# Kernel tuning notes

Measured on AMD Instinct MI355X. Metric: run time of the kernel, lower is better.

Reference implementation:

```python
import jax, jax.numpy as jnp
import numpy as np

N_NODES = 100000
N_EDGES = 1600000
NFEAT = 128
NHID = 128
NCLASS = 40


def gcn_conv(x, W, b, src, dst, n_nodes):
    """PyG-style GCNConv: x' = D^{-1/2}(A+I)D^{-1/2} (x W) + b."""
    h = x @ W  # [N, out]
    loop = jnp.arange(n_nodes, dtype=src.dtype)
    s = jnp.concatenate([src, loop])  # add self-loops
    d = jnp.concatenate([dst, loop])
    deg = jax.ops.segment_sum(jnp.ones_like(s, dtype=h.dtype), d, num_segments=n_nodes)
    dinv = jnp.where(deg > 0, jax.lax.rsqrt(deg), 0.0)
    norm = dinv[s] * dinv[d]  # [E+N]
    msg = h[s] * norm[:, None]  # gather + scale
    out = jax.ops.segment_sum(msg, d, num_segments=n_nodes)  # scatter-add
    return out + b


def setup_inputs() -> dict:
    key = jax.random.key(0)
    ks = jax.random.split(key, 6)
    x = jax.random.normal(ks[0], (N_NODES, NFEAT), dtype=jnp.float32)
    edge_index = jax.random.randint(ks[1], (2, N_EDGES), 0, N_NODES, dtype=jnp.int64)
    sc1 = 1.0 / np.sqrt(NFEAT)
    sc2 = 1.0 / np.sqrt(NHID)
    W1 = jax.random.normal(ks[2], (NFEAT, NHID), dtype=jnp.float32) * sc1
    b1 = jnp.zeros((NHID,), dtype=jnp.float32)
    Wm = jax.random.normal(ks[3], (NHID, NHID), dtype=jnp.float32) * sc2
    bm = jnp.zeros((NHID,), dtype=jnp.float32)
    W2 = jax.random.normal(ks[4], (NHID, NCLASS), dtype=jnp.float32) * sc2
    b2 = jnp.zeros((NCLASS,), dtype=jnp.float32)
    return {"x": x, "edge_index": edge_index, "W1": W1, "b1": b1,
            "Wm": Wm, "bm": bm, "W2": W2, "b2": b2}


def reference(x, edge_index, W1, b1, Wm, bm, W2, b2):
    # StandGCNX forward, eval mode (dropout = identity)
    src, dst = edge_index[0], edge_index[1]
    n = x.shape[0]
    h = jax.nn.relu(gcn_conv(x, W1, b1, src, dst, n))
    h = jax.nn.relu(gcn_conv(h, Wm, bm, src, dst, n))
    out = gcn_conv(h, W2, b2, src, dst, n)
    return out
```

## Files before the change

kernel.cpp:

```cpp
#include <hip/hip_runtime.h>
#include <hip/hip_bf16.h>

typedef __attribute__((ext_vector_type(8))) short bf16x8;
typedef __attribute__((ext_vector_type(4))) float f32x4;

__device__ __forceinline__ ushort bf16rne(float f) {
    uint u = __float_as_uint(f);
    return (ushort)((u + 0x7fffu + ((u >> 16) & 1u)) >> 16);
}
__device__ __forceinline__ void unpack2(uint p, float& a, float& b) {
    a = __uint_as_float(p << 16);
    b = __uint_as_float(p & 0xffff0000u);
}


__global__ __launch_bounds__(256) void k_pre1(const float* __restrict__ W1,
                                              const float* __restrict__ Wm,
                                              const float* __restrict__ W2,
                                              ushort* __restrict__ w1t,
                                              ushort* __restrict__ wmt,
                                              ushort* __restrict__ w2t,
                                              const int* __restrict__ dst,
                                              int* __restrict__ bcnt, int E) {
    __shared__ int hist[512];
    int b = blockIdx.x;
    int t = threadIdx.x;
    if (b < 152) {
        if (b < 64) {
            int i = b * 256 + t; int k = i >> 7, n = i & 127;
            w1t[n * 128 + k] = bf16rne(W1[k * 128 + n]);
        } else if (b < 128) {
            int i = (b - 64) * 256 + t; int k = i >> 7, n = i & 127;
            wmt[n * 128 + k] = bf16rne(Wm[k * 128 + n]);
        } else {
            int i = (b - 128) * 256 + t;
            if (i < 6144) {
                int n = i >> 7, k = i & 127;
                w2t[n * 128 + k] = (n < 40) ? bf16rne(W2[k * 40 + n]) : (ushort)0;
            }
        }
        return;
    }
    hist[t] = 0; hist[t + 256] = 0;
    __syncthreads();
    int off = (b - 152) * 4096;
    int cnt = min(4096, E - off);
    for (int i = t; i < cnt; i += 256) atomicAdd(&hist[dst[off + i] >> 8], 1);
    __syncthreads();
    if (hist[t]) atomicAdd(&bcnt[t], hist[t]);
    if (hist[t + 256]) atomicAdd(&bcnt[t + 256], hist[t + 256]);
}

__global__ void k_bscan(const int* __restrict__ bcnt, int* __restrict__ bbase,
                        int* __restrict__ bcur, int nbuck) {
    __shared__ int s[512];
    int t = threadIdx.x;
    s[t] = (t < nbuck) ? bcnt[t] : 0;
    __syncthreads();
    for (int d = 1; d < 512; d <<= 1) {
        int u = (t >= d) ? s[t - d] : 0;
        __syncthreads();
        if (t >= d) s[t] += u;
        __syncthreads();
    }
    int excl = (t == 0) ? 0 : s[t - 1];
    bbase[t] = excl;
    if (t < nbuck) bcur[t] = excl;
    if (t == 511) bbase[512] = s[511];
}


__global__ __launch_bounds__(256) void k_pack_gemm(const int* __restrict__ src,
                                                   const int* __restrict__ dst,
                                                   int* __restrict__ bcur,
                                                   uint* __restrict__ pairbuf,
                                                   int E, int nbuck, int ntile,
                                                   const float* __restrict__ A,
                                                   const ushort* __restrict__ Wt,
                                                   ushort* __restrict__ C, int M) {
    __shared__ int hist[512];
    __shared__ int scn[512];
    __shared__ int cur[512];
    __shared__ int gbase[512];
    __shared__ uint sorted[4096];
    int t = threadIdx.x;
    if ((int)blockIdx.x >= ntile) {
        int blk = blockIdx.x - ntile;
        int wave = t >> 6, lane = t & 63;
        int m16 = lane & 15, quad = lane >> 4;
        int rowA = blk * 64 + wave * 16 + m16;
        int rA = min(rowA, M - 1);
        const float4* A4 = (const float4*)A;

        f32x4 acc[8];
#pragma unroll
        for (int i = 0; i < 8; i++) acc[i] = (f32x4){0.f, 0.f, 0.f, 0.f};
#pragma unroll
        for (int it = 0; it < 4; it++) {
            float4 f0 = A4[(size_t)rA * 32 + 8 * it + 2 * quad];
            float4 f1 = A4[(size_t)rA * 32 + 8 * it + 2 * quad + 1];
            bf16x8 af;
            af[0] = (short)bf16rne(f0.x); af[1] = (short)bf16rne(f0.y);
            af[2] = (short)bf16rne(f0.z); af[3] = (short)bf16rne(f0.w);
            af[4] = (short)bf16rne(f1.x); af[5] = (short)bf16rne(f1.y);
            af[6] = (short)bf16rne(f1.z); af[7] = (short)bf16rne(f1.w);
#pragma unroll
            for (int nt = 0; nt < 8; nt++) {
                bf16x8 bfr = *(const bf16x8*)(Wt + (size_t)(nt * 16 + m16) * 128 + it * 32 + quad * 8);
                acc[nt] = __builtin_amdgcn_mfma_f32_16x16x32_bf16(af, bfr, acc[nt], 0, 0, 0);
            }
        }
        int rowBase = blk * 64 + wave * 16 + quad * 4;
#pragma unroll
        for (int nt = 0; nt < 8; nt++) {
            int col = nt * 16 + m16;
#pragma unroll
            for (int r = 0; r < 4; r++) {
                int row = rowBase + r;
                if (row < M) C[(size_t)row * 128 + col] = bf16rne(acc[nt][r]);
            }
        }
        return;
    }
    int off = blockIdx.x * 4096;
    int cnt = min(4096, E - off);
    hist[t] = 0; hist[t + 256] = 0;
    __syncthreads();
    for (int i = t; i < cnt; i += 256) {
        int b = dst[off + i] >> 8;
        atomicAdd(&hist[b], 1);
    }
    __syncthreads();
    scn[t] = hist[t]; scn[t + 256] = hist[t + 256];
    __syncthreads();
    for (int d = 1; d < 256; d <<= 1) {
        int u0 = (t >= d) ? scn[t - d] : 0;
        int u1 = (t >= d) ? scn[256 + t - d] : 0;
        __syncthreads();
        if (t >= d) { scn[t] += u0; scn[256 + t] += u1; }
        __syncthreads();
    }
    int tot0 = scn[255];
    scn[256 + t] += tot0;
    __syncthreads();
    cur[t] = (t == 0) ? 0 : scn[t - 1];
    cur[t + 256] = scn[t + 255];
    if (t < nbuck && hist[t] > 0) gbase[t] = atomicAdd(&bcur[t], hist[t]);
    int t2 = t + 256;
    if (t2 < nbuck && hist[t2] > 0) gbase[t2] = atomicAdd(&bcur[t2], hist[t2]);
    __syncthreads();
    for (int i = t; i < cnt; i += 256) {
        int d = dst[off + i];
        int s = src[off + i];
        int b = d >> 8;
        int pos = atomicAdd(&cur[b], 1);
        sorted[pos] = ((uint)(d & 255) << 24) | (uint)s;
    }
    __syncthreads();
    int wid = t >> 6, lane = t & 63;
    for (int b = wid; b < nbuck; b += 4) {
        int n = hist[b];
        if (n == 0) continue;
        int ls = (b == 0) ? 0 : scn[b - 1];
        int gb = gbase[b];
        for (int j = lane; j < n; j += 64)
            pairbuf[gb + j] = sorted[ls + j];
    }
}

#define CSR_CAP 5632
__global__ __launch_bounds__(256) void k_csrbuild(const uint* __restrict__ pairbuf,
                                                  const int* __restrict__ bbase,
                                                  int* __restrict__ rowptr,
                                                  float* __restrict__ dinv,
                                                  int* __restrict__ csr,
                                                  int N, int nbuck) {
    __shared__ int lhist[256];
    __shared__ int scn[256];
    __shared__ int lcur[256];
    __shared__ int lcsr[CSR_CAP];
    int b = blockIdx.x;
    int base = b << 8;
    int nn = min(256, N - base);
    int lo = bbase[b], hi = bbase[b + 1];
    int cnt = hi - lo;
    int t = threadIdx.x;
    lhist[t] = 0;
    __syncthreads();
    for (int i = t; i < cnt; i += 256) atomicAdd(&lhist[pairbuf[lo + i] >> 24], 1);
    __syncthreads();
    int mydeg = lhist[t];
    scn[t] = mydeg;
    __syncthreads();
    for (int d = 1; d < 256; d <<= 1) {
        int u = (t >= d) ? scn[t - d] : 0;
        __syncthreads();
        if (t >= d) scn[t] += u;
        __syncthreads();
    }
    int excl = (t == 0) ? 0 : scn[t - 1];
    lcur[t] = excl;
    if (t < nn) {
        rowptr[base + t] = lo + excl;
        dinv[base + t] = rsqrtf((float)(mydeg + 1));
    }
    if (b == nbuck - 1 && t == 0) rowptr[N] = hi;
    __syncthreads();
    if (cnt <= CSR_CAP) {
        for (int i = t; i < cnt; i += 256) {
            uint p = pairbuf[lo + i];
            int pos = atomicAdd(&lcur[p >> 24], 1);
            lcsr[pos] = (int)(p & 0xFFFFFFu);
        }
        __syncthreads();
        for (int i = t; i < cnt; i += 256) csr[lo + i] = lcsr[i];
    } else {
        for (int i = t; i < cnt; i += 256) {
            uint p = pairbuf[lo + i];
            int pos = lo + atomicAdd(&lcur[p >> 24], 1);
            csr[pos] = (int)(p & 0xFFFFFFu);
        }
    }
}


template <bool EDGE_W>
__device__ __forceinline__ void agg_issue8(const uint* __restrict__ g32, int lane,
                                           int sidx, int swi, int j,
                                           uint P[8], float W[8]) {
#pragma unroll
    for (int k = 0; k < 8; k++) {
        int s = __builtin_amdgcn_readlane(sidx, j + k);
        W[k] = __int_as_float(__builtin_amdgcn_readlane(swi, j + k));
        P[k] = g32[(size_t)s * 64 + lane];
    }
}
__device__ __forceinline__ void agg_consume8(const uint P[8], const float W[8],
                                             float& a0, float& a1) {
#pragma unroll
    for (int k = 0; k < 8; k++) {
        float u, v;
        unpack2(P[k], u, v);
        a0 += u * W[k];
        a1 += v * W[k];
    }
}

template <int NT, bool EDGE_W>
__device__ __forceinline__ void fused_agg_gemm(const ushort* __restrict__ g,
                                               const float* __restrict__ dinv,
                                               const int* __restrict__ rowptr,
                                               const int* __restrict__ csr,
                                               const float* __restrict__ bias,
                                               const ushort* __restrict__ Wt,
                                               ushort* __restrict__ C,
                                               int M, int ccols) {
    __shared__ ushort hs[32][136];
    __shared__ int nextNode;
    int t = threadIdx.x;
    if (t == 0) nextNode = 0;
    __syncthreads();
    int lane = t & 63;
    const uint* g32 = (const uint*)g;
    float2 bb = ((const float2*)bias)[lane];

    for (;;) {
        int idx0 = 0;
        if (lane == 0) idx0 = atomicAdd(&nextNode, 2);
        idx0 = __builtin_amdgcn_readfirstlane(idx0);
        if (idx0 >= 32) break;
        int ndA = min(blockIdx.x * 32 + idx0, M - 1);
        int ndB = min(blockIdx.x * 32 + idx0 + 1, M - 1);
        float dnA = dinv[ndA], dnB = dinv[ndB];
        int e0A = rowptr[ndA], e1A = rowptr[ndA + 1];
        int e0B = rowptr[ndB], e1B = rowptr[ndB + 1];
        uint pSA = g32[(size_t)ndA * 64 + lane];
        uint pSB = g32[(size_t)ndB * 64 + lane];
        float a0, a1, b0, b1;
        {
            float u, v;
            unpack2(pSA, u, v);
            if (EDGE_W) { a0 = u * dnA; a1 = v * dnA; } else { a0 = u; a1 = v; }
            unpack2(pSB, u, v);
            if (EDGE_W) { b0 = u * dnB; b1 = v * dnB; } else { b0 = u; b1 = v; }
        }
        int baseA = e0A, baseB = e0B;
        while (baseA < e1A || baseB < e1B) {
            int ncA = e1A - baseA; if (ncA > 64) ncA = 64;
            int ncB = e1B - baseB; if (ncB > 64) ncB = 64;
            int sidxA = 0, swiA = 0, sidxB = 0, swiB = 0;
            if (lane < ncA) {
                sidxA = csr[baseA + lane];
                swiA = EDGE_W ? __float_as_int(dinv[sidxA]) : 0x3f800000;
            }
            if (lane < ncB) {
                sidxB = csr[baseB + lane];
                swiB = EDGE_W ? __float_as_int(dinv[sidxB]) : 0x3f800000;
            }
            int nc8A = (ncA + 7) & ~7;
            int nc8B = (ncB + 7) & ~7;
            int jA = 0, jB = 0;
            while (jA < nc8A && jB < nc8B) {
                uint PA[8], PB[8];
                float WA[8], WB[8];
                agg_issue8<EDGE_W>(g32, lane, sidxA, swiA, jA, PA, WA);
                agg_issue8<EDGE_W>(g32, lane, sidxB, swiB, jB, PB, WB);
                agg_consume8(PA, WA, a0, a1);
                agg_consume8(PB, WB, b0, b1);
                jA += 8; jB += 8;
            }
            while (jA < nc8A) {
                uint PA[8]; float WA[8];
                agg_issue8<EDGE_W>(g32, lane, sidxA, swiA, jA, PA, WA);
                agg_consume8(PA, WA, a0, a1);
                jA += 8;
            }
            while (jB < nc8B) {
                uint PB[8]; float WB[8];
                agg_issue8<EDGE_W>(g32, lane, sidxB, swiB, jB, PB, WB);
                agg_consume8(PB, WB, b0, b1);
                jB += 8;
            }
            baseA += ncA;
            baseB += ncB;
        }
        float o0 = fmaxf(a0 * dnA + bb.x, 0.f);
        float o1 = fmaxf(a1 * dnA + bb.y, 0.f);
        float o2 = fmaxf(b0 * dnB + bb.x, 0.f);
        float o3 = fmaxf(b1 * dnB + bb.y, 0.f);
        uint qA = (uint)bf16rne(o0) | ((uint)bf16rne(o1) << 16);
        uint qB = (uint)bf16rne(o2) | ((uint)bf16rne(o3) << 16);
        *(uint*)&hs[idx0][lane * 2] = qA;
        *(uint*)&hs[idx0 + 1][lane * 2] = qB;
    }
    __syncthreads();

    int wave = t >> 6, lane6 = t & 63;
    int m16 = lane6 & 15, quad = lane6 >> 4;
    int rowHalf = wave & 1;
    int ntHalf = wave >> 1;
    constexpr int NTH = (NT + 1) / 2;
    int ntStart = ntHalf * NTH;
    int ntEnd = ntHalf ? NT : NTH;

    f32x4 acc[NTH];
#pragma unroll
    for (int i = 0; i < NTH; i++) acc[i] = (f32x4){0.f, 0.f, 0.f, 0.f};
#pragma unroll
    for (int it = 0; it < 4; it++) {
        bf16x8 af = *(const bf16x8*)&hs[rowHalf * 16 + m16][it * 32 + quad * 8];
        for (int nt = ntStart; nt < ntEnd; nt++) {
            bf16x8 bfr = *(const bf16x8*)(Wt + (size_t)(nt * 16 + m16) * 128 + it * 32 + quad * 8);
            acc[nt - ntStart] = __builtin_amdgcn_mfma_f32_16x16x32_bf16(af, bfr, acc[nt - ntStart], 0, 0, 0);
        }
    }
    int rowBase = blockIdx.x * 32 + rowHalf * 16 + quad * 4;
    float dnv[4];
#pragma unroll
    for (int r = 0; r < 4; r++) dnv[r] = dinv[min(rowBase + r, M - 1)];
    for (int nt = ntStart; nt < ntEnd; nt++) {
        int col = nt * 16 + m16;
        if (col >= ccols) continue;
#pragma unroll
        for (int r = 0; r < 4; r++) {
            int row = rowBase + r;
            if (row < M) C[(size_t)row * ccols + col] = bf16rne(acc[nt - ntStart][r] * dnv[r]);
        }
    }
}

__global__ __launch_bounds__(256) void k_fusedA(const ushort* __restrict__ g,
                                                const float* __restrict__ dinv,
                                                const int* __restrict__ rowptr,
                                                const int* __restrict__ csr,
                                                const float* __restrict__ bias,
                                                const ushort* __restrict__ Wt,
                                                ushort* __restrict__ C, int M) {
    fused_agg_gemm<8, true>(g, dinv, rowptr, csr, bias, Wt, C, M, 128);
}

__global__ __launch_bounds__(256) void k_fusedB(const ushort* __restrict__ g,
                                                const float* __restrict__ dinv,
                                                const int* __restrict__ rowptr,
                                                const int* __restrict__ csr,
                                                const float* __restrict__ bias,
                                                const ushort* __restrict__ Wt,
                                                ushort* __restrict__ C, int M) {
    fused_agg_gemm<3, false>(g, dinv, rowptr, csr, bias, Wt, C, M, 40);
}


__global__ __launch_bounds__(256) void k_agg40_b(const ushort* __restrict__ g3,
                                                 const float* __restrict__ dinv,
                                                 const int* __restrict__ rowptr,
                                                 const int* __restrict__ csr,
                                                 const float* __restrict__ bias,
                                                 float* __restrict__ out, int N) {
    int t = threadIdx.x;
    if (t >= 250) return;
    int grp = t / 10;
    int l = t - grp * 10;
    int node = blockIdx.x * 25 + grp;
    if (node >= N) return;
    const uint2* gp = (const uint2*)g3;
    float dn = dinv[node];
    float a0, a1, a2, a3;
    {
        uint2 p = gp[(size_t)node * 10 + l];
        unpack2(p.x, a0, a1);
        unpack2(p.y, a2, a3);
    }
    int e0 = rowptr[node], e1 = rowptr[node + 1];
    int e = e0;
    for (; e + 4 <= e1; e += 4) {
        int s0 = csr[e], s1 = csr[e + 1], s2 = csr[e + 2], s3 = csr[e + 3];
        uint2 p0 = gp[(size_t)s0 * 10 + l];
        uint2 p1 = gp[(size_t)s1 * 10 + l];
        uint2 p2 = gp[(size_t)s2 * 10 + l];
        uint2 p3 = gp[(size_t)s3 * 10 + l];
        float u, v;
        unpack2(p0.x, u, v); a0 += u; a1 += v;
        unpack2(p0.y, u, v); a2 += u; a3 += v;
        unpack2(p1.x, u, v); a0 += u; a1 += v;
        unpack2(p1.y, u, v); a2 += u; a3 += v;
        unpack2(p2.x, u, v); a0 += u; a1 += v;
        unpack2(p2.y, u, v); a2 += u; a3 += v;
        unpack2(p3.x, u, v); a0 += u; a1 += v;
        unpack2(p3.y, u, v); a2 += u; a3 += v;
    }
    for (; e < e1; e++) {
        int s = csr[e];
        uint2 p = gp[(size_t)s * 10 + l];
        float u, v;
        unpack2(p.x, u, v); a0 += u; a1 += v;
        unpack2(p.y, u, v); a2 += u; a3 += v;
    }
    float4 bb = ((const float4*)bias)[l];
    float4 o;
    o.x = a0 * dn + bb.x;
    o.y = a1 * dn + bb.y;
    o.z = a2 * dn + bb.z;
    o.w = a3 * dn + bb.w;
    ((float4*)out)[(size_t)node * 10 + l] = o;
}


extern "C" void kernel_launch(void* const* d_in, const int* in_sizes, int n_in,
                              void* d_out, int out_size, void* d_ws, size_t ws_size,
                              hipStream_t stream) {
    const float* x  = (const float*)d_in[0];
    const int* eidx = (const int*)d_in[1];
    const float* W1 = (const float*)d_in[2];
    const float* b1 = (const float*)d_in[3];
    const float* Wm = (const float*)d_in[4];
    const float* bm = (const float*)d_in[5];
    const float* W2 = (const float*)d_in[6];
    const float* b2 = (const float*)d_in[7];
    float* out = (float*)d_out;

    int N = in_sizes[0] / 128;
    int E = in_sizes[1] / 2;
    const int* src = eidx;
    const int* dst = eidx + E;
    int nbuck = (N + 255) >> 8;
    int ntile = (E + 4095) / 4096;

    char* ws = (char*)d_ws;
    size_t off = 0;
    auto alloc = [&](size_t bytes) -> void* {
        void* p = ws + off;
        off += (bytes + 255) & ~(size_t)255;
        return p;
    };
    float*  dinv    = (float*)alloc((size_t)N * 4);
    int*    rowptr  = (int*)alloc(((size_t)N + 1) * 4);
    int*    csr     = (int*)alloc((size_t)E * 4);
    uint*   pairbuf = (uint*)alloc((size_t)E * 4);
    int*    bcnt    = (int*)alloc(512 * 4);
    int*    bbase   = (int*)alloc(513 * 4);
    int*    bcur    = (int*)alloc(512 * 4);
    ushort* w1t     = (ushort*)alloc(128 * 128 * 2);
    ushort* wmt     = (ushort*)alloc(128 * 128 * 2);
    ushort* w2t     = (ushort*)alloc(48 * 128 * 2);
    ushort* gbuf    = (ushort*)alloc((size_t)N * 128 * 2);
    ushort* gbuf2   = (ushort*)alloc((size_t)N * 128 * 2);
    ushort* g3      = (ushort*)alloc((size_t)N * 40 * 2);

    int gblk64 = (N + 63) / 64;
    int gblk32 = (N + 31) / 32;

    hipMemsetAsync(bcnt, 0, 512 * 4, stream);
    k_pre1<<<152 + ntile, 256, 0, stream>>>(W1, Wm, W2, w1t, wmt, w2t, dst, bcnt, E);
    k_bscan<<<1, 512, 0, stream>>>(bcnt, bbase, bcur, nbuck);
    k_pack_gemm<<<ntile + gblk64, 256, 0, stream>>>(src, dst, bcur, pairbuf, E, nbuck,
                                                    ntile, x, w1t, gbuf, N);
    k_csrbuild<<<nbuck, 256, 0, stream>>>(pairbuf, bbase, rowptr, dinv, csr, N, nbuck);
    k_fusedA<<<gblk32, 256, 0, stream>>>(gbuf, dinv, rowptr, csr, b1, wmt, gbuf2, N);
    k_fusedB<<<gblk32, 256, 0, stream>>>(gbuf2, dinv, rowptr, csr, bm, w2t, g3, N);
    k_agg40_b<<<(N + 24) / 25, 256, 0, stream>>>(g3, dinv, rowptr, csr, b2, out, N);
}
```

Baseline: 357.6 us.

## Statically assign node pairs per wave and batch-load CSR indices for paired nodes

```diff
diff --git a/kernel.cpp b/kernel.cpp
--- a/kernel.cpp
+++ b/kernel.cpp
@@ -225,24 +225,79 @@
 
 
 template <bool EDGE_W>
-__device__ __forceinline__ void agg_issue8(const uint* __restrict__ g32, int lane,
-                                           int sidx, int swi, int j,
-                                           uint P[8], float W[8]) {
+__device__ __forceinline__ void batch8(const uint* __restrict__ g32, int lane,
+                                       int creg, int wreg, int j, int lim,
+                                       float& x0, float& x1) {
+    uint P[8]; float W[8];
 #pragma unroll
     for (int k = 0; k < 8; k++) {
-        int s = __builtin_amdgcn_readlane(sidx, j + k);
-        W[k] = __int_as_float(__builtin_amdgcn_readlane(swi, j + k));
+        int idx = j + k;
+        int cl = idx < 63 ? idx : 63;
+        int s = __builtin_amdgcn_readlane(creg, cl);
+        float w = EDGE_W ? __int_as_float(__builtin_amdgcn_readlane(wreg, cl)) : 1.0f;
+        W[k] = (idx < lim) ? w : 0.0f;
         P[k] = g32[(size_t)s * 64 + lane];
     }
-}
-__device__ __forceinline__ void agg_consume8(const uint P[8], const float W[8],
-                                             float& a0, float& a1) {
 #pragma unroll
     for (int k = 0; k < 8; k++) {
-        float u, v;
-        unpack2(P[k], u, v);
-        a0 += u * W[k];
-        a1 += v * W[k];
+        float u, v; unpack2(P[k], u, v);
+        x0 += u * W[k]; x1 += v * W[k];
+    }
+}
+
+template <bool EDGE_W>
+__device__ __forceinline__ void batch8x2(const uint* __restrict__ g32, int lane,
+                                         int cA, int wA, int jA, int limA,
+                                         float& a0, float& a1,
+                                         int cB, int wB, int jB, int limB,
+                                         float& b0, float& b1) {
+    uint PA[8], PB[8]; float WA[8], WB[8];
+#pragma unroll
+    for (int k = 0; k < 8; k++) {
+        int idx = jA + k;
+        int cl = idx < 63 ? idx : 63;
+        int s = __builtin_amdgcn_readlane(cA, cl);
+        float w = EDGE_W ? __int_as_float(__builtin_amdgcn_readlane(wA, cl)) : 1.0f;
+        WA[k] = (idx < limA) ? w : 0.0f;
+        PA[k] = g32[(size_t)s * 64 + lane];
+    }
+#pragma unroll
+    for (int k = 0; k < 8; k++) {
+        int idx = jB + k;
+        int cl = idx < 63 ? idx : 63;
+        int s = __builtin_amdgcn_readlane(cB, cl);
+        float w = EDGE_W ? __int_as_float(__builtin_amdgcn_readlane(wB, cl)) : 1.0f;
+        WB[k] = (idx < limB) ? w : 0.0f;
+        PB[k] = g32[(size_t)s * 64 + lane];
+    }
+#pragma unroll
+    for (int k = 0; k < 8; k++) {
+        float u, v; unpack2(PA[k], u, v);
+        a0 += u * WA[k]; a1 += v * WA[k];
+    }
+#pragma unroll
+    for (int k = 0; k < 8; k++) {
+        float u, v; unpack2(PB[k], u, v);
+        b0 += u * WB[k]; b1 += v * WB[k];
+    }
+}
+
+template <bool EDGE_W>
+__device__ __forceinline__ void agg_node_chunked(const uint* __restrict__ g32,
+                                                 const int* __restrict__ csr,
+                                                 const float* __restrict__ dinv,
+                                                 int lane, int e0, int e1,
+                                                 float& x0, float& x1) {
+    for (int base = e0; base < e1; base += 64) {
+        int nc = e1 - base; if (nc > 64) nc = 64;
+        int sidx = 0, swi = 0;
+        if (lane < nc) {
+            sidx = csr[base + lane];
+            if (EDGE_W) swi = __float_as_int(dinv[sidx]);
+        }
+        int nc8 = (nc + 7) & ~7;
+        for (int j = 0; j < nc8; j += 8)
+            batch8<EDGE_W>(g32, lane, sidx, swi, j, nc, x0, x1);
     }
 }
 
@@ -256,73 +311,88 @@
                                                ushort* __restrict__ C,
                                                int M, int ccols) {
     __shared__ ushort hs[32][136];
-    __shared__ int nextNode;
     int t = threadIdx.x;
-    if (t == 0) nextNode = 0;
-    __syncthreads();
     int lane = t & 63;
+    int wave = t >> 6;
     const uint* g32 = (const uint*)g;
     float2 bb = ((const float2*)bias)[lane];
 
-    for (;;) {
-        int idx0 = 0;
-        if (lane == 0) idx0 = atomicAdd(&nextNode, 2);
-        idx0 = __builtin_amdgcn_readfirstlane(idx0);
-        if (idx0 >= 32) break;
-        int ndA = min(blockIdx.x * 32 + idx0, M - 1);
-        int ndB = min(blockIdx.x * 32 + idx0 + 1, M - 1);
-        float dnA = dinv[ndA], dnB = dinv[ndB];
-        int e0A = rowptr[ndA], e1A = rowptr[ndA + 1];
-        int e0B = rowptr[ndB], e1B = rowptr[ndB + 1];
-        uint pSA = g32[(size_t)ndA * 64 + lane];
-        uint pSB = g32[(size_t)ndB * 64 + lane];
+    int nodeBase = blockIdx.x * 32 + wave * 8;
+    int nd_l = min(nodeBase + lane, M - 1);
+
+    uint srow[8];
+#pragma unroll
+    for (int i = 0; i < 8; i++) {
+        int nd = __builtin_amdgcn_readlane(nd_l, i);
+        srow[i] = g32[(size_t)nd * 64 + lane];
+    }
+    int e0_l = 0, e1_l = 0; float dn_l = 0.f;
+    if (lane < 8) {
+        e0_l = rowptr[nd_l];
+        e1_l = rowptr[nd_l + 1];
+        dn_l = dinv[nd_l];
+    }
+    int c0 = 0, c1 = 0, c2 = 0, c3 = 0;
+    int w0 = 0, w1 = 0, w2 = 0, w3 = 0;
+    int sp0, sp1, sp2, sp3, Ls0, Ls1, Ls2, Ls3;
+    sp0 = __builtin_amdgcn_readlane(e0_l, 0);
+    Ls0 = __builtin_amdgcn_readlane(e1_l, 1) - sp0;
+    sp1 = __builtin_amdgcn_readlane(e0_l, 2);
+    Ls1 = __builtin_amdgcn_readlane(e1_l, 3) - sp1;
+    sp2 = __builtin_amdgcn_readlane(e0_l, 4);
+    Ls2 = __builtin_amdgcn_readlane(e1_l, 5) - sp2;
+    sp3 = __builtin_amdgcn_readlane(e0_l, 6);
+    Ls3 = __builtin_amdgcn_readlane(e1_l, 7) - sp3;
+    if (Ls0 <= 64 && lane < Ls0) c0 = csr[sp0 + lane];
+    if (Ls1 <= 64 && lane < Ls1) c1 = csr[sp1 + lane];
+    if (Ls2 <= 64 && lane < Ls2) c2 = csr[sp2 + lane];
+    if (Ls3 <= 64 && lane < Ls3) c3 = csr[sp3 + lane];
+    if (EDGE_W) {
+        if (Ls0 <= 64 && lane < Ls0) w0 = __float_as_int(dinv[c0]);
+        if (Ls1 <= 64 && lane < Ls1) w1 = __float_as_int(dinv[c1]);
+        if (Ls2 <= 64 && lane < Ls2) w2 = __float_as_int(dinv[c2]);
+        if (Ls3 <= 64 && lane < Ls3) w3 = __float_as_int(dinv[c3]);
+    }
+    int cp[4] = {c0, c1, c2, c3};
+    int wp[4] = {w0, w1, w2, w3};
+    int spp[4] = {sp0, sp1, sp2, sp3};
+    int Lsp[4] = {Ls0, Ls1, Ls2, Ls3};
+
+#pragma unroll
+    for (int p = 0; p < 4; p++) {
+        int iA = 2 * p, iB = 2 * p + 1;
+        int eA0 = __builtin_amdgcn_readlane(e0_l, iA);
+        int eA1 = __builtin_amdgcn_readlane(e1_l, iA);
+        int eB0 = __builtin_amdgcn_readlane(e0_l, iB);
+        int eB1 = __builtin_amdgcn_readlane(e1_l, iB);
+        float dnA = __int_as_float(__builtin_amdgcn_readlane(__float_as_int(dn_l), iA));
+        float dnB = __int_as_float(__builtin_amdgcn_readlane(__float_as_int(dn_l), iB));
         float a0, a1, b0, b1;
         {
             float u, v;
-            unpack2(pSA, u, v);
+            unpack2(srow[2 * p], u, v);
             if (EDGE_W) { a0 = u * dnA; a1 = v * dnA; } else { a0 = u; a1 = v; }
-            unpack2(pSB, u, v);
+            unpack2(srow[2 * p + 1], u, v);
             if (EDGE_W) { b0 = u * dnB; b1 = v * dnB; } else { b0 = u; b1 = v; }
         }
-        int baseA = e0A, baseB = e0B;
-        while (baseA < e1A || baseB < e1B) {
-            int ncA = e1A - baseA; if (ncA > 64) ncA = 64;
-            int ncB = e1B - baseB; if (ncB > 64) ncB = 64;
-            int sidxA = 0, swiA = 0, sidxB = 0, swiB = 0;
-            if (lane < ncA) {
-                sidxA = csr[baseA + lane];
-                swiA = EDGE_W ? __float_as_int(dinv[sidxA]) : 0x3f800000;
-            }
-            if (lane < ncB) {
-                sidxB = csr[baseB + lane];
-                swiB = EDGE_W ? __float_as_int(dinv[sidxB]) : 0x3f800000;
-            }
-            int nc8A = (ncA + 7) & ~7;
-            int nc8B = (ncB + 7) & ~7;
-            int jA = 0, jB = 0;
-            while (jA < nc8A && jB < nc8B) {
-                uint PA[8], PB[8];
-                float WA[8], WB[8];
-                agg_issue8<EDGE_W>(g32, lane, sidxA, swiA, jA, PA, WA);
-                agg_issue8<EDGE_W>(g32, lane, sidxB, swiB, jB, PB, WB);
-                agg_consume8(PA, WA, a0, a1);
-                agg_consume8(PB, WB, b0, b1);
+        if (Lsp[p] <= 64) {
+            int offA = eA0 - spp[p];
+            int offB = eB0 - spp[p];
+            int nA = eA1 - eA0, nB = eB1 - eB0;
+            int limA = offA + nA, limB = offB + nB;
+            int jA = offA, jB = offB;
+            int jAend = offA + ((nA + 7) & ~7);
+            int jBend = offB + ((nB + 7) & ~7);
+            while (jA < jAend && jB < jBend) {
+                batch8x2<EDGE_W>(g32, lane, cp[p], wp[p], jA, limA, a0, a1,
+                                 cp[p], wp[p], jB, limB, b0, b1);
                 jA += 8; jB += 8;
             }
-            while (jA < nc8A) {
-                uint PA[8]; float WA[8];
-                agg_issue8<EDGE_W>(g32, lane, sidxA, swiA, jA, PA, WA);
-                agg_consume8(PA, WA, a0, a1);
-                jA += 8;
-            }
-            while (jB < nc8B) {
-                uint PB[8]; float WB[8];
-                agg_issue8<EDGE_W>(g32, lane, sidxB, swiB, jB, PB, WB);
-                agg_consume8(PB, WB, b0, b1);
-                jB += 8;
-            }
-            baseA += ncA;
-            baseB += ncB;
+            while (jA < jAend) { batch8<EDGE_W>(g32, lane, cp[p], wp[p], jA, limA, a0, a1); jA += 8; }
+            while (jB < jBend) { batch8<EDGE_W>(g32, lane, cp[p], wp[p], jB, limB, b0, b1); jB += 8; }
+        } else {
+            agg_node_chunked<EDGE_W>(g32, csr, dinv, lane, eA0, eA1, a0, a1);
+            agg_node_chunked<EDGE_W>(g32, csr, dinv, lane, eB0, eB1, b0, b1);
         }
         float o0 = fmaxf(a0 * dnA + bb.x, 0.f);
         float o1 = fmaxf(a1 * dnA + bb.y, 0.f);
@@ -330,15 +400,15 @@
         float o3 = fmaxf(b1 * dnB + bb.y, 0.f);
         uint qA = (uint)bf16rne(o0) | ((uint)bf16rne(o1) << 16);
         uint qB = (uint)bf16rne(o2) | ((uint)bf16rne(o3) << 16);
-        *(uint*)&hs[idx0][lane * 2] = qA;
-        *(uint*)&hs[idx0 + 1][lane * 2] = qB;
-    }
-    __syncthreads();
-
-    int wave = t >> 6, lane6 = t & 63;
+        *(uint*)&hs[wave * 8 + 2 * p][lane * 2] = qA;
+        *(uint*)&hs[wave * 8 + 2 * p + 1][lane * 2] = qB;
+    }
+    __syncthreads();
+
+    int wv = t >> 6, lane6 = t & 63;
     int m16 = lane6 & 15, quad = lane6 >> 4;
-    int rowHalf = wave & 1;
-    int ntHalf = wave >> 1;
+    int rowHalf = wv & 1;
+    int ntHalf = wv >> 1;
     constexpr int NTH = (NT + 1) / 2;
     int ntStart = ntHalf * NTH;
     int ntEnd = ntHalf ? NT : NTH;
```

New measurement: 359.5 us. About the same (+0.5%).
